# Optimization experiments

Hardware: AMD Instinct MI355X
Metric: run time of the kernel (lower is better)

The kernel has to match this reference:

```python
import jax, jax.numpy as jnp
import numpy as np

NEG = -1000000000.0  # mask value used by the original module

def setup_inputs() -> dict:
    key = jax.random.key(0)
    kq, kk, kv, kl = jax.random.split(key, 4)
    B, Lq, Lk, D, Dv = 16, 2048, 2048, 64, 64
    q = jax.random.normal(kq, (B, Lq, D), dtype=jnp.float32)
    k = jax.random.normal(kk, (B, Lk, D), dtype=jnp.float32)
    v = jax.random.normal(kv, (B, Lk, Dv), dtype=jnp.float32)
    valid_len = jax.random.randint(kl, (B, Lq), 0, Lk, dtype=jnp.int32)
    return {"q": q, "k": k, "v": v, "valid_len": valid_len}

def reference(q, k, v, valid_len):
    # scores: [B, Lq, Lk]  (NOTE: original module does NOT scale by sqrt(d))
    scores = jnp.einsum('bqd,bkd->bqk', q, k)
    Lk = k.shape[1]
    # per-(batch,query) valid length masking over the key dimension
    mask = jnp.arange(Lk, dtype=valid_len.dtype)[None, None, :] < valid_len[:, :, None]
    scores = jnp.where(mask, scores, NEG)
    attn = jax.nn.softmax(scores, axis=-1)
    # dropout p=0.0 -> identity
    return jnp.einsum('bqk,bkv->bqv', attn, v)
```

## Files before the change

kernel.cpp:

```cpp
#include <hip/hip_runtime.h>

typedef _Float16 f16;
typedef __attribute__((ext_vector_type(8))) _Float16 f16x8;
typedef __attribute__((ext_vector_type(4))) _Float16 f16x4;
typedef __attribute__((ext_vector_type(4))) float f32x4;

#define NB 16
#define LSEQ 2048
#define DIM 64
#define KVB 64
#define QT 128
#define NQT (LSEQ / QT)
#define NT (LSEQ / KVB)
#define PITCH 72
#define LOG2E 1.44269504088896340736f

__device__ inline f16x4 pkcvt(const f32x4 x) {
    auto a = __builtin_amdgcn_cvt_pkrtz(x[0], x[1]);
    auto b = __builtin_amdgcn_cvt_pkrtz(x[2], x[3]);
    f16x4 t; t[0]=(f16)a[0]; t[1]=(f16)a[1]; t[2]=(f16)b[0]; t[3]=(f16)b[1];
    return t;
}

__device__ inline void gload16(const void* g, void* l) {
    __builtin_amdgcn_global_load_lds(
        (const __attribute__((address_space(1))) unsigned int*)g,
        (__attribute__((address_space(3))) unsigned int*)l, 16, 0, 0);
}

__global__ __launch_bounds__(256) void prep(
    const float* __restrict__ kg, const float* __restrict__ vg,
    const int* __restrict__ vlg,
    f16* __restrict__ k16, f16* __restrict__ v16, int* __restrict__ perm)
{
    const int tid = threadIdx.x;
    if (blockIdx.x < NB * NT) {
        const int bt = blockIdx.x;
        const int b = bt >> 5, t = bt & 31;
        const float* kb_ = kg + ((size_t)b * LSEQ + t * KVB) * DIM;
        const float* vb_ = vg + ((size_t)b * LSEQ + t * KVB) * DIM;
        f16* kd = k16 + (size_t)bt * (KVB * DIM);
        f16* vd = v16 + (size_t)bt * (KVB * DIM);
#pragma unroll
        for (int it = 0; it < 4; ++it) {
            int cc = tid + it * 256;
            int row = cc >> 4, c4 = (cc & 15) * 4;
            f32x4 x = *(const f32x4*)(kb_ + row * DIM + c4);
            *(f16x4*)(kd + row * 64 + (c4 ^ ((row & 7) * 8))) = pkcvt(x);
        }
        int kb4 = tid & 15, dvb = tid >> 4;
        f32x4 rr[4];
#pragma unroll
        for (int i = 0; i < 4; ++i)
            rr[i] = *(const f32x4*)(vb_ + (size_t)(kb4 * 4 + i) * DIM + dvb * 4);
#pragma unroll
        for (int j = 0; j < 4; ++j) {
            int dv = dvb * 4 + j;
            f32x4 col = {rr[0][j], rr[1][j], rr[2][j], rr[3][j]};
            *(f16x4*)(vd + dv * 64 + ((kb4 * 4) ^ ((dv & 7) * 8))) = pkcvt(col);
        }
    } else {
        const int b = blockIdx.x - NB * NT;
        __shared__ int hist[NT + 1];
        __shared__ int base[NT + 1];
        if (tid <= NT) hist[tid] = 0;
        __syncthreads();
        for (int q = tid; q < LSEQ; q += 256) {
            int vl = vlg[b * LSEQ + q];
            int t = (vl == 0) ? NT : ((vl + KVB - 1) >> 6);
            atomicAdd(&hist[t], 1);
        }
        __syncthreads();
        if (tid == 0) {
            int acc = 0;
            for (int t = NT; t >= 0; --t) { base[t] = acc; acc += hist[t]; }
        }
        __syncthreads();
        for (int q = tid; q < LSEQ; q += 256) {
            int vl = vlg[b * LSEQ + q];
            int t = (vl == 0) ? NT : ((vl + KVB - 1) >> 6);
            int pos = atomicAdd(&base[t], 1);
            perm[b * LSEQ + pos] = q;
        }
    }
}

__global__ __launch_bounds__(256, 3) void attn_fwd(
    const float* __restrict__ qg, const int* __restrict__ vlg,
    const f16* __restrict__ k16, const f16* __restrict__ v16,
    float* __restrict__ outg, const int* __restrict__ perm,
    f16* __restrict__ opart, float* __restrict__ mlg, int S)
{
    __shared__ alignas(16) f16 kbuf[2][KVB * 64];
    __shared__ alignas(16) f16 vbuf[2][DIM * 64];
    __shared__ alignas(16) f16 pld[4 * 16 * PITCH];
    __shared__ int wmax[4];

    const int tid  = threadIdx.x;
    const int wid  = tid >> 6;
    const int lane = tid & 63;
    const int r    = lane & 15;
    const int hi   = lane >> 4;

    const int bid = blockIdx.x;
    const int nbs = NB * S;
    const int qt  = bid / nbs;
    const int rem = bid - qt * nbs;
    const int b   = rem / S;
    const int s   = rem - b * S;
    const int qw  = qt * QT + wid * 16;

    const int qidxA = perm[b * LSEQ + qw + r];
    const int qidxB = perm[b * LSEQ + qw + 64 + r];
    const int vlA   = vlg[b * LSEQ + qidxA];
    const int vlB   = vlg[b * LSEQ + qidxB];

    int tq = max((vlA == 0) ? NT : ((vlA + KVB - 1) >> 6),
                 (vlB == 0) ? NT : ((vlB + KVB - 1) >> 6));
    tq = max(tq, __shfl_xor(tq, 1));
    tq = max(tq, __shfl_xor(tq, 2));
    tq = max(tq, __shfl_xor(tq, 4));
    tq = max(tq, __shfl_xor(tq, 8));
    if (lane == 0) wmax[wid] = tq;
    __syncthreads();
    const int maxt = max(max(wmax[0], wmax[1]), max(wmax[2], wmax[3]));

    auto wave_min = [&](int v) {
        v = min(v, __shfl_xor(v, 1));
        v = min(v, __shfl_xor(v, 2));
        v = min(v, __shfl_xor(v, 4));
        v = min(v, __shfl_xor(v, 8));
        return v;
    };
    const int vminA = wave_min(vlA);
    const int vminB = wave_min(vlB);

    auto load_q = [&](int qidx, f16x8* qf) {
        const float* qrow = qg + ((size_t)(b * LSEQ + qidx)) * DIM;
#pragma unroll
        for (int ks = 0; ks < 2; ++ks) {
            f32x4 x = *(const f32x4*)(qrow + ks * 32 + hi * 8);
            f32x4 y = *(const f32x4*)(qrow + ks * 32 + hi * 8 + 4);
            f32x4 xs = {x[0]*LOG2E, x[1]*LOG2E, x[2]*LOG2E, x[3]*LOG2E};
            f32x4 ys = {y[0]*LOG2E, y[1]*LOG2E, y[2]*LOG2E, y[3]*LOG2E};
            f16x4 lo = pkcvt(xs), hh = pkcvt(ys);
            f16x8 t;
            t[0]=lo[0]; t[1]=lo[1]; t[2]=lo[2]; t[3]=lo[3];
            t[4]=hh[0]; t[5]=hh[1]; t[6]=hh[2]; t[7]=hh[3];
            qf[ks] = t;
        }
    };
    f16x8 qfA[2], qfB[2];
    load_q(qidxA, qfA);
    load_q(qidxB, qfB);

    float mA = -INFINITY, mB = -INFINITY;
    float lA = 0.0f, lB = 0.0f;
    f32x4 oA[4], oB[4];
#pragma unroll
    for (int dt = 0; dt < 4; ++dt) { oA[dt] = f32x4{0,0,0,0}; oB[dt] = f32x4{0,0,0,0}; }

    f16* pw = pld + wid * (16 * PITCH);
    const f16* kt_base = k16 + (size_t)b * (NT * KVB * DIM);
    const f16* vt_base = v16 + (size_t)b * (NT * KVB * DIM);
    const int swz = (r & 7) * 8;

    auto stage = [&](int bi, int t) {
        const char* ks = (const char*)(kt_base + (size_t)t * 4096);
        const char* vs = (const char*)(vt_base + (size_t)t * 4096);
        char* kd = (char*)&kbuf[bi][0];
        char* vd = (char*)&vbuf[bi][0];
        gload16(ks + tid * 16,        kd + tid * 16);
        gload16(ks + 4096 + tid * 16, kd + 4096 + tid * 16);
        gload16(vs + tid * 16,        vd + tid * 16);
        gload16(vs + 4096 + tid * 16, vd + 4096 + tid * 16);
    };

    auto do_frag = [&](const f16x8* qf, int vl, int vmin,
                       float& m_run, float& l_run, f32x4* o,
                       int kv0, const f16* kb_, const f16* vb_) {
        f32x4 st[4];
        __builtin_amdgcn_s_setprio(1);
#pragma unroll
        for (int kt = 0; kt < 4; ++kt) {
            f32x4 acc = f32x4{0,0,0,0};
#pragma unroll
            for (int ks = 0; ks < 2; ++ks) {
                f16x8 kf = *(const f16x8*)(&kb_[(kt * 16 + r) * 64 + ((ks * 32 + hi * 8) ^ swz)]);
                acc = __builtin_amdgcn_mfma_f32_16x16x32_f16(kf, qf[ks], acc, 0, 0, 0);
            }
            st[kt] = acc;
        }
        __builtin_amdgcn_s_setprio(0);

        float lanemax = -INFINITY;
        if (kv0 + KVB > vmin) {
#pragma unroll
            for (int kt = 0; kt < 4; ++kt)
#pragma unroll
                for (int g = 0; g < 4; ++g) {
                    int key = kv0 + kt * 16 + hi * 4 + g;
                    float sv = (key < vl) ? st[kt][g] : -1e9f;
                    st[kt][g] = sv;
                    lanemax = fmaxf(lanemax, sv);
                }
        } else {
#pragma unroll
            for (int kt = 0; kt < 4; ++kt)
#pragma unroll
                for (int g = 0; g < 4; ++g)
                    lanemax = fmaxf(lanemax, st[kt][g]);
        }

        if (__any(lanemax > m_run + 8.0f)) {
            float tmax = lanemax;
            tmax = fmaxf(tmax, __shfl_xor(tmax, 16));
            tmax = fmaxf(tmax, __shfl_xor(tmax, 32));
            float m_new = fmaxf(m_run, tmax);
            float scale = exp2f(m_run - m_new);
            l_run *= scale;
            m_run = m_new;
#pragma unroll
            for (int g = 0; g < 4; ++g) {
                float sc = __shfl(scale, hi * 4 + g);
#pragma unroll
                for (int dt = 0; dt < 4; ++dt) o[dt][g] *= sc;
            }
        }

#pragma unroll
        for (int kt = 0; kt < 4; ++kt) {
            f16x4 pv;
#pragma unroll
            for (int g = 0; g < 4; ++g) {
                float p = exp2f(st[kt][g] - m_run);
                l_run += p;
                pv[g] = (f16)p;
            }
            *(f16x4*)(pw + r * PITCH + kt * 16 + hi * 4) = pv;
        }

        __builtin_amdgcn_s_setprio(1);
#pragma unroll
        for (int ks = 0; ks < 2; ++ks) {
            f16x8 pa = *(const f16x8*)(pw + r * PITCH + ks * 32 + hi * 8);
#pragma unroll
            for (int dt = 0; dt < 4; ++dt) {
                f16x8 vf = *(const f16x8*)(&vb_[(dt * 16 + r) * 64 + ((ks * 32 + hi * 8) ^ swz)]);
                o[dt] = __builtin_amdgcn_mfma_f32_16x16x32_f16(pa, vf, o[dt], 0, 0, 0);
            }
        }
        __builtin_amdgcn_s_setprio(0);
    };

    if (s < maxt) stage(0, s);
    int c = 0;
    for (int tt = s; tt < maxt; tt += S) {
        __syncthreads();
        if (tt + S < maxt) stage(c ^ 1, tt + S);
        const int kv0 = tt * KVB;
        do_frag(qfA, vlA, vminA, mA, lA, oA, kv0, &kbuf[c][0], &vbuf[c][0]);
        do_frag(qfB, vlB, vminB, mB, lB, oB, kv0, &kbuf[c][0], &vbuf[c][0]);
        c ^= 1;
    }

    auto epi = [&](float m_run, float l_run, f32x4* o, int qidx) {
        l_run += __shfl_xor(l_run, 16);
        l_run += __shfl_xor(l_run, 32);
        if (S == 1) {
            float inv = 1.0f / l_run;
#pragma unroll
            for (int g = 0; g < 4; ++g) {
                float iv = __shfl(inv, hi * 4 + g);
                int   qo = __shfl(qidx, hi * 4 + g);
                float* ob = outg + ((size_t)(b * LSEQ + qo)) * DIM;
#pragma unroll
                for (int dt = 0; dt < 4; ++dt)
                    ob[dt * 16 + r] = o[dt][g] * iv;
            }
        } else {
            f16* obase = opart + ((size_t)s * NB * LSEQ + (size_t)b * LSEQ) * DIM;
#pragma unroll
            for (int g = 0; g < 4; ++g) {
                int qo = __shfl(qidx, hi * 4 + g);
                f16* ob = obase + (size_t)qo * DIM;
#pragma unroll
                for (int dt = 0; dt < 4; ++dt)
                    ob[dt * 16 + r] = (f16)o[dt][g];
            }
            if (hi == 0) {
                size_t mi = ((size_t)s * NB * LSEQ + (size_t)b * LSEQ + qidx) * 2;
                mlg[mi]     = m_run;
                mlg[mi + 1] = l_run;
            }
        }
    };
    epi(mA, lA, oA, qidxA);
    epi(mB, lB, oB, qidxB);
}

__global__ void merge_k(const f16* __restrict__ opart, const float* __restrict__ mlg,
                        float* __restrict__ outg, int S)
{
    const int gt = blockIdx.x * 256 + threadIdx.x;
    const size_t base = (size_t)gt * 4;
    const size_t qg = base >> 6;
    float M = -INFINITY;
    for (int s = 0; s < S; ++s)
        M = fmaxf(M, mlg[((size_t)s * NB * LSEQ + qg) * 2]);
    float den = 0.f;
    f32x4 acc = {0.f, 0.f, 0.f, 0.f};
    for (int s = 0; s < S; ++s) {
        size_t mi = ((size_t)s * NB * LSEQ + qg) * 2;
        float w = exp2f(mlg[mi] - M);
        den += w * mlg[mi + 1];
        f16x4 ov = *(const f16x4*)(opart + (size_t)s * (NB * LSEQ * DIM) + base);
        acc[0] += w * (float)ov[0]; acc[1] += w * (float)ov[1];
        acc[2] += w * (float)ov[2]; acc[3] += w * (float)ov[3];
    }
    float inv = 1.0f / den;
    f32x4 res = {acc[0]*inv, acc[1]*inv, acc[2]*inv, acc[3]*inv};
    *(f32x4*)(outg + base) = res;
}

extern "C" void kernel_launch(void* const* d_in, const int* in_sizes, int n_in,
                              void* d_out, int out_size, void* d_ws, size_t ws_size,
                              hipStream_t stream) {
    const float* q  = (const float*)d_in[0];
    const float* k  = (const float*)d_in[1];
    const float* v  = (const float*)d_in[2];
    const int*   vl = (const int*)d_in[3];
    float* out = (float*)d_out;

    const size_t perm_b = (size_t)NB * LSEQ * sizeof(int);
    const size_t kv_b   = (size_t)NB * LSEQ * DIM * sizeof(f16);
    auto need = [&](int S) {
        return perm_b + 2 * kv_b
             + (size_t)S * NB * LSEQ * 2 * sizeof(float)
             + (size_t)S * NB * LSEQ * DIM * sizeof(f16);
    };
    int S;
    if      (ws_size >= need(4)) S = 4;
    else if (ws_size >= need(2)) S = 2;
    else                         S = 1;

    int*   perm  = (int*)d_ws;
    f16*   k16   = (f16*)((char*)d_ws + perm_b);
    f16*   v16   = (f16*)((char*)d_ws + perm_b + kv_b);
    float* mlg   = (float*)((char*)d_ws + perm_b + 2 * kv_b);
    f16*   opart = (f16*)((char*)d_ws + perm_b + 2 * kv_b
                          + (size_t)S * NB * LSEQ * 2 * sizeof(float));

    prep<<<NB * NT + NB, 256, 0, stream>>>(k, v, vl, k16, v16, perm);

    attn_fwd<<<dim3(NQT * NB * S), dim3(256), 0, stream>>>(
        q, vl, k16, v16, out, perm, opart, mlg, S);

    if (S > 1) {
        const int mthreads = NB * LSEQ * DIM / 4;
        merge_k<<<dim3(mthreads / 256), dim3(256), 0, stream>>>(opart, mlg, out, S);
    }
}
```

Baseline: 51.16 us.

## Permute K rows in prep so P stays in registers for PV MFMA

Rows within each K tile are reordered in the prep kernel with a kappa permutation, so the QK^T MFMA output lands in exactly the register layout the PV MFMA needs as its A operand. This removes the per-wave P round trip through LDS (write, then read back) and frees that shared memory. The mask key index is adjusted to match. Occupancy is raised to 4 blocks per CU, and the block-to-(batch, split) mapping is changed to batch-fastest ordering. The risks are register pressure at the higher occupancy bound and subtle mistakes in the permuted masking.

```diff
diff --git a/kernel.cpp b/kernel.cpp
--- a/kernel.cpp
+++ b/kernel.cpp
@@ -12,7 +12,6 @@
 #define QT 128
 #define NQT (LSEQ / QT)
 #define NT (LSEQ / KVB)
-#define PITCH 72
 #define LOG2E 1.44269504088896340736f
 
 __device__ inline f16x4 pkcvt(const f32x4 x) {
@@ -26,6 +25,11 @@
     __builtin_amdgcn_global_load_lds(
         (const __attribute__((address_space(1))) unsigned int*)g,
         (__attribute__((address_space(3))) unsigned int*)l, 16, 0, 0);
+}
+
+__device__ __host__ inline int kappa(int p) {
+    int kt = p >> 4, hi = (p >> 2) & 3, g = p & 3;
+    return ((kt & 1) << 5) + (hi << 3) + ((kt >> 1) << 2) + g;
 }
 
 __global__ __launch_bounds__(256) void prep(
@@ -35,8 +39,8 @@
 {
     const int tid = threadIdx.x;
     if (blockIdx.x < NB * NT) {
-        const int bt = blockIdx.x;
-        const int b = bt >> 5, t = bt & 31;
+        const int b = blockIdx.x & 15, t = blockIdx.x >> 4;
+        const int bt = b * NT + t;
         const float* kb_ = kg + ((size_t)b * LSEQ + t * KVB) * DIM;
         const float* vb_ = vg + ((size_t)b * LSEQ + t * KVB) * DIM;
         f16* kd = k16 + (size_t)bt * (KVB * DIM);
@@ -45,7 +49,7 @@
         for (int it = 0; it < 4; ++it) {
             int cc = tid + it * 256;
             int row = cc >> 4, c4 = (cc & 15) * 4;
-            f32x4 x = *(const f32x4*)(kb_ + row * DIM + c4);
+            f32x4 x = *(const f32x4*)(kb_ + kappa(row) * DIM + c4);
             *(f16x4*)(kd + row * 64 + (c4 ^ ((row & 7) * 8))) = pkcvt(x);
         }
         int kb4 = tid & 15, dvb = tid >> 4;
@@ -85,7 +89,7 @@
     }
 }
 
-__global__ __launch_bounds__(256, 3) void attn_fwd(
+__global__ __launch_bounds__(256, 4) void attn_fwd(
     const float* __restrict__ qg, const int* __restrict__ vlg,
     const f16* __restrict__ k16, const f16* __restrict__ v16,
     float* __restrict__ outg, const int* __restrict__ perm,
@@ -93,7 +97,6 @@
 {
     __shared__ alignas(16) f16 kbuf[2][KVB * 64];
     __shared__ alignas(16) f16 vbuf[2][DIM * 64];
-    __shared__ alignas(16) f16 pld[4 * 16 * PITCH];
     __shared__ int wmax[4];
 
     const int tid  = threadIdx.x;
@@ -106,8 +109,8 @@
     const int nbs = NB * S;
     const int qt  = bid / nbs;
     const int rem = bid - qt * nbs;
-    const int b   = rem / S;
-    const int s   = rem - b * S;
+    const int s   = rem >> 4;
+    const int b   = rem & 15;
     const int qw  = qt * QT + wid * 16;
 
     const int qidxA = perm[b * LSEQ + qw + r];
@@ -125,15 +128,15 @@
     __syncthreads();
     const int maxt = max(max(wmax[0], wmax[1]), max(wmax[2], wmax[3]));
 
-    auto wave_min = [&](int v) {
+    auto rmin = [&](int v) {
         v = min(v, __shfl_xor(v, 1));
         v = min(v, __shfl_xor(v, 2));
         v = min(v, __shfl_xor(v, 4));
         v = min(v, __shfl_xor(v, 8));
         return v;
     };
-    const int vminA = wave_min(vlA);
-    const int vminB = wave_min(vlB);
+    const int vminA = rmin(vlA);
+    const int vminB = rmin(vlB);
 
     auto load_q = [&](int qidx, f16x8* qf) {
         const float* qrow = qg + ((size_t)(b * LSEQ + qidx)) * DIM;
@@ -160,7 +163,6 @@
 #pragma unroll
     for (int dt = 0; dt < 4; ++dt) { oA[dt] = f32x4{0,0,0,0}; oB[dt] = f32x4{0,0,0,0}; }
 
-    f16* pw = pld + wid * (16 * PITCH);
     const f16* kt_base = k16 + (size_t)b * (NT * KVB * DIM);
     const f16* vt_base = v16 + (size_t)b * (NT * KVB * DIM);
     const int swz = (r & 7) * 8;
@@ -199,7 +201,7 @@
             for (int kt = 0; kt < 4; ++kt)
 #pragma unroll
                 for (int g = 0; g < 4; ++g) {
-                    int key = kv0 + kt * 16 + hi * 4 + g;
+                    int key = kv0 + ((kt & 1) << 5) + (hi << 3) + ((kt >> 1) << 2) + g;
                     float sv = (key < vl) ? st[kt][g] : -1e9f;
                     st[kt][g] = sv;
                     lanemax = fmaxf(lanemax, sv);
@@ -228,28 +230,24 @@
             }
         }
 
-#pragma unroll
-        for (int kt = 0; kt < 4; ++kt) {
-            f16x4 pv;
+        f16x8 pa[2];
+#pragma unroll
+        for (int kt = 0; kt < 4; ++kt)
 #pragma unroll
             for (int g = 0; g < 4; ++g) {
                 float p = exp2f(st[kt][g] - m_run);
                 l_run += p;
-                pv[g] = (f16)p;
-            }
-            *(f16x4*)(pw + r * PITCH + kt * 16 + hi * 4) = pv;
-        }
+                pa[kt & 1][((kt >> 1) << 2) + g] = (f16)p;
+            }
 
         __builtin_amdgcn_s_setprio(1);
 #pragma unroll
-        for (int ks = 0; ks < 2; ++ks) {
-            f16x8 pa = *(const f16x8*)(pw + r * PITCH + ks * 32 + hi * 8);
+        for (int ks = 0; ks < 2; ++ks)
 #pragma unroll
             for (int dt = 0; dt < 4; ++dt) {
                 f16x8 vf = *(const f16x8*)(&vb_[(dt * 16 + r) * 64 + ((ks * 32 + hi * 8) ^ swz)]);
-                o[dt] = __builtin_amdgcn_mfma_f32_16x16x32_f16(pa, vf, o[dt], 0, 0, 0);
-            }
-        }
+                o[dt] = __builtin_amdgcn_mfma_f32_16x16x32_f16(pa[ks], vf, o[dt], 0, 0, 0);
+            }
         __builtin_amdgcn_s_setprio(0);
     };
 
```

Result: faster. 46.17 us (-9.8%).
